# Performance work log

Hardware: AMD Instinct MI355X
Metric: run time of the kernel (lower is better)

The kernel has to match this reference:

```python
import jax, jax.numpy as jnp
import numpy as np

N_NODES = 200000
N_EDGES = 3200000
N_GRAPHS = 2000
N_MAX = 256   # max nodes per graph for dense batching (mean ~100)
K = 30        # SortAggregation k


def setup_inputs() -> dict:
    key = jax.random.key(0)
    ks = jax.random.split(key, 12)
    x = jax.random.normal(ks[0], (N_NODES, 128), jnp.float32)
    edge_index = jax.random.randint(ks[1], (2, N_EDGES), 0, N_NODES, dtype=jnp.int32)
    batch = jnp.sort(jax.random.randint(ks[2], (N_NODES,), 0, N_GRAPHS, dtype=jnp.int32))
    def lin(k, i, o):
        return (jax.random.normal(k, (i, o), jnp.float32) / np.sqrt(i)).astype(jnp.float32)
    return {
        'x': x, 'edge_index': edge_index, 'batch': batch,
        'W1': lin(ks[3], 128, 32), 'b1': jnp.zeros(32, jnp.float32),
        'W2': lin(ks[4], 32, 32),  'b2': jnp.zeros(32, jnp.float32),
        'W3': lin(ks[5], 32, 32),  'b3': jnp.zeros(32, jnp.float32),
        'W4': lin(ks[6], 32, 1),   'b4': jnp.zeros(1, jnp.float32),
        'cw5': (jax.random.normal(ks[7], (16, 1, 97), jnp.float32) / np.sqrt(97)).astype(jnp.float32),
        'cb5': jnp.zeros(16, jnp.float32),
        'cw6': (jax.random.normal(ks[8], (32, 16, 5), jnp.float32) / np.sqrt(80)).astype(jnp.float32),
        'cb6': jnp.zeros(32, jnp.float32),
        'fw1': lin(ks[9], 352, 128), 'fb1': jnp.zeros(128, jnp.float32),
        'fw2': lin(ks[10], 128, 10), 'fb2': jnp.zeros(10, jnp.float32),
    }


def _gcn_conv(h, W, b, src, dst, emask):
    # PyG GCNConv: remove self-loops handled via emask (weight 0), then add
    # self-loops weight 1; symmetric normalization D^{-1/2}(A+I)D^{-1/2} X W + b
    deg = jax.ops.segment_sum(emask, dst, num_segments=N_NODES) + 1.0  # + self loop
    dis = jax.lax.rsqrt(deg)  # deg >= 1 always, no inf
    norm = dis[src] * dis[dst] * emask  # [E]
    hw = h @ W                          # [N, out]
    agg = jax.ops.segment_sum(hw[src] * norm[:, None], dst, num_segments=N_NODES)
    agg = agg + hw * (dis * dis)[:, None]  # self-loop message
    return agg + b


def _sort_pool(x, batch):
    # PyG SortAggregation(k): dense-batch with fill = min-1, sort each graph by
    # last feature channel (descending), keep top-k rows, zero out padding, flatten.
    N, D = x.shape
    ones = jnp.ones((N,), jnp.int32)
    counts = jax.ops.segment_sum(ones, batch, num_segments=N_GRAPHS)
    offsets = jnp.concatenate([jnp.zeros((1,), jnp.int32), jnp.cumsum(counts)[:-1]])
    pos = jnp.arange(N, dtype=jnp.int32) - offsets[batch]  # batch is sorted
    fill = x.min() - 1.0
    dense = jnp.full((N_GRAPHS, N_MAX, D), fill, x.dtype).at[batch, pos].set(x)
    perm = jnp.argsort(-dense[:, :, -1], axis=1)            # descending by last channel
    dense = jnp.take_along_axis(dense, perm[:, :, None], axis=1)[:, :K]  # [G, K, D]
    dense = jnp.where(dense == fill, 0.0, dense)
    return dense.reshape(N_GRAPHS, K * D)


def _conv1d(x, w, b, stride):
    y = jax.lax.conv_general_dilated(x, w, window_strides=(stride,), padding='VALID',
                                     dimension_numbers=('NCH', 'OIH', 'NCH'))
    return y + b[None, :, None]


def reference(x, edge_index, batch, W1, b1, W2, b2, W3, b3, W4, b4,
              cw5, cb5, cw6, cb6, fw1, fb1, fw2, fb2):
    src, dst = edge_index[0], edge_index[1]
    emask = (src != dst).astype(x.dtype)  # remove_self_loops

    x1 = jnp.tanh(_gcn_conv(x,  W1, b1, src, dst, emask))
    x2 = jnp.tanh(_gcn_conv(x1, W2, b2, src, dst, emask))
    x3 = jnp.tanh(_gcn_conv(x2, W3, b3, src, dst, emask))
    x4 = jnp.tanh(_gcn_conv(x3, W4, b4, src, dst, emask))
    h = jnp.concatenate([x1, x2, x3, x4], axis=-1)  # [N, 97]

    p = _sort_pool(h, batch)                 # [G, 30*97]
    p = p[:, None, :]                        # [G, 1, 2910]
    p = jax.nn.relu(_conv1d(p, cw5, cb5, 97))  # [G, 16, 30]
    G = p.shape[0]
    p = p.reshape(G, 16, 15, 2).max(axis=-1)   # MaxPool1d(2,2) -> [G, 16, 15]
    p = jax.nn.relu(_conv1d(p, cw6, cb6, 1))   # [G, 32, 11]
    p = p.reshape(G, -1)                       # [G, 352]
    out = jax.nn.relu(p @ fw1 + fb1)           # dropout is identity at inference
    return jax.nn.log_softmax(out @ fw2 + fb2, axis=-1)
```

## Files before the change

### kernel.cpp

```cpp
#include <hip/hip_runtime.h>

#define N_NODESC 200000
#define N_EDGESC 3200000
#define N_GRAPHSC 2000
#define NMAXG 256
#define TOPK 30
#define DCAT 97
#define POOLW (TOPK*DCAT)
#define BUCKW 512
#define NBUCK ((N_NODESC+BUCKW-1)/BUCKW)
#define CAP 10240
#define PCHUNK 4096
#define NPBLK ((N_EDGESC+PCHUNK-1)/PCHUNK)

typedef int  iv4 __attribute__((ext_vector_type(4)));
typedef float fv4 __attribute__((ext_vector_type(4)));

__global__ __launch_bounds__(256) void k_part(const int* __restrict__ src, const int* __restrict__ dst,
                                              const int* __restrict__ batch, int* __restrict__ gcount,
                                              int* __restrict__ bcur, unsigned* __restrict__ pairbuf){
  __shared__ int hcnt[NBUCK];
  __shared__ int hbase[NBUCK];
  int blk = blockIdx.x, t = threadIdx.x;
  int nd = blk*256 + t;
  if (nd < N_NODESC) atomicAdd(&gcount[batch[nd]],1);
  int e0 = blk*PCHUNK;
  int e1 = e0 + PCHUNK; if (e1 > N_EDGESC) e1 = N_EDGESC;
  for (int i=t;i<NBUCK;i+=256) hcnt[i]=0;
  unsigned pk[16]; unsigned meta[16];
  __syncthreads();
  #pragma unroll
  for (int i=0;i<4;i++){
    int e = e0 + i*1024 + t*4;
    if (e < e1){
      iv4 d4 = __builtin_nontemporal_load((const iv4*)(dst+e));
      iv4 s4 = __builtin_nontemporal_load((const iv4*)(src+e));
      #pragma unroll
      for (int k=0;k<4;k++){
        int d = (k==0)?d4.x:(k==1)?d4.y:(k==2)?d4.z:d4.w;
        int s = (k==0)?s4.x:(k==1)?s4.y:(k==2)?s4.z:s4.w;
        if (s!=d){
          int bk = d>>9;
          int pl = atomicAdd(&hcnt[bk],1);
          pk[i*4+k]   = ((unsigned)(d&511)<<18)|(unsigned)s;
          meta[i*4+k] = ((unsigned)bk<<13)|(unsigned)pl;
        } else meta[i*4+k] = 0xFFFFFFFFu;
      }
    } else {
      #pragma unroll
      for (int k=0;k<4;k++) meta[i*4+k] = 0xFFFFFFFFu;
    }
  }
  __syncthreads();
  for (int i=t;i<NBUCK;i+=256){
    int c = hcnt[i];
    hbase[i] = c ? (i*CAP + atomicAdd(&bcur[i],c)) : 0;
  }
  __syncthreads();
  #pragma unroll
  for (int k=0;k<16;k++){
    unsigned m = meta[k];
    if (m != 0xFFFFFFFFu){
      int bk = (int)(m>>13);
      int pos = hbase[bk] + (int)(m & 0x1FFFu);
      if (pos < (bk+1)*CAP) pairbuf[pos] = pk[k];
    }
  }
}

__global__ __launch_bounds__(512) void k_bsort(const unsigned* __restrict__ pairbuf, const int* __restrict__ bcur,
                                               int* __restrict__ degc, int* __restrict__ offs,
                                               float* __restrict__ dis, int* __restrict__ csr){
  __shared__ int lcsr[CAP];
  __shared__ int lcnt[512];
  __shared__ int lofs[512];
  __shared__ int lcur[512];
  __shared__ int red[512];
  int b = blockIdx.x, t = threadIdx.x;
  int cnt_b = bcur[b]; if (cnt_b > CAP) cnt_b = CAP;
  int pv = 0;
  if (t < b){ int c = bcur[t]; if (c>CAP) c=CAP; pv = c; }
  red[t]=pv; __syncthreads();
  for (int off=256;off>0;off>>=1){ if (t<off) red[t]+=red[t+off]; __syncthreads(); }
  int base = red[0];
  const unsigned* pb = pairbuf + (size_t)b*CAP;
  lcnt[t]=0; __syncthreads();
  for (int i=t;i<cnt_b;i+=512) atomicAdd(&lcnt[pb[i]>>18],1);
  __syncthreads();
  lofs[t]=lcnt[t]; __syncthreads();
  for (int off=1;off<512;off<<=1){
    int u = (t>=off)? lofs[t-off] : 0;
    __syncthreads();
    lofs[t]+=u;
    __syncthreads();
  }
  int excl = lofs[t]-lcnt[t];
  int node = b*BUCKW + t;
  if (node < N_NODESC){
    degc[node] = lcnt[t];
    offs[node] = base + excl;
    dis[node]  = rsqrtf((float)lcnt[t] + 1.0f);
  }
  lcur[t]=excl;
  __syncthreads();
  for (int i=t;i<cnt_b;i+=512){
    unsigned v = pb[i];
    int p = atomicAdd(&lcur[v>>18],1);
    lcsr[p] = (int)(v & 0x3FFFFu);
  }
  __syncthreads();
  for (int i=t;i<cnt_b;i+=512) csr[base+i]=lcsr[i];
}

template<int KIN>
__global__ __launch_bounds__(256) void k_mm(const float* __restrict__ X, const float* __restrict__ W,
                                            const float* __restrict__ dis, float* __restrict__ out){
  __shared__ float xs[256*33];
  int r0 = blockIdx.x*256;
  int t = threadIdx.x;
  int r = r0 + t;
  float acc[32];
  #pragma unroll
  for (int f=0;f<32;f++) acc[f]=0.f;
  for (int kc=0; kc<KIN; kc+=32){
    __syncthreads();
    #pragma unroll
    for (int it=0; it<8; it++){
      int idx = it*256 + t;
      int row = idx>>3, c4 = idx&7;
      int gr = r0 + row;
      fv4 v = {0.f,0.f,0.f,0.f};
      if (gr < N_NODESC) v = __builtin_nontemporal_load((const fv4*)(X + (size_t)gr*KIN + kc + c4*4));
      int bofs = row*33 + c4*4;
      xs[bofs]=v.x; xs[bofs+1]=v.y; xs[bofs+2]=v.z; xs[bofs+3]=v.w;
    }
    __syncthreads();
    const float* w0 = W + kc*32;
    const float* xrow = xs + t*33;
    #pragma unroll
    for (int k=0;k<32;k++){
      float xv = xrow[k];
      #pragma unroll
      for (int f=0;f<32;f++) acc[f] = fmaf(xv, w0[k*32+f], acc[f]);
    }
  }
  if (r >= N_NODESC) return;
  float d = dis[r];
  float4* op = (float4*)(out + (size_t)r*32);
  #pragma unroll
  for (int f4=0;f4<8;f4++)
    op[f4] = make_float4(acc[4*f4]*d, acc[4*f4+1]*d, acc[4*f4+2]*d, acc[4*f4+3]*d);
}

__global__ void k_mm4(const float* __restrict__ X, const float* __restrict__ W, const float* __restrict__ dis, float* __restrict__ out){
  int r = blockIdx.x*256+threadIdx.x;
  if (r>=N_NODESC) return;
  const float4* xr = (const float4*)(X + (size_t)r*32);
  float acc=0.f;
  #pragma unroll
  for (int k4=0;k4<8;k4++){
    float4 xv = xr[k4];
    acc = fmaf(xv.x, W[k4*4+0], acc);
    acc = fmaf(xv.y, W[k4*4+1], acc);
    acc = fmaf(xv.z, W[k4*4+2], acc);
    acc = fmaf(xv.w, W[k4*4+3], acc);
  }
  out[r]=acc*dis[r];
}

__global__ __launch_bounds__(256) void k_agg(const float* __restrict__ hws, const int* __restrict__ csr,
                      const int* __restrict__ off, const int* __restrict__ cnt,
                      const float* __restrict__ dis, const float* __restrict__ bias,
                      float* __restrict__ out){
  int t = blockIdx.x*256 + threadIdx.x;
  int n = t>>5;
  if (n>=N_NODESC) return;
  int f = t&31;
  int beg = off[n], c = cnt[n];
  float a0=0.f,a1=0.f,a2=0.f,a3=0.f,a4=0.f,a5=0.f,a6=0.f,a7=0.f;
  for (int base=0; base<c; base+=32){
    int m = c-base; if (m>32) m=32;
    int idx = (f<m)? csr[beg+base+f] : 0;
    int j=0;
    for (; j+8<=m; j+=8){
      int s0=__shfl(idx,j,32),   s1=__shfl(idx,j+1,32),
          s2=__shfl(idx,j+2,32), s3=__shfl(idx,j+3,32),
          s4=__shfl(idx,j+4,32), s5=__shfl(idx,j+5,32),
          s6=__shfl(idx,j+6,32), s7=__shfl(idx,j+7,32);
      float v0=hws[(size_t)s0*32+f];
      float v1=hws[(size_t)s1*32+f];
      float v2=hws[(size_t)s2*32+f];
      float v3=hws[(size_t)s3*32+f];
      float v4=hws[(size_t)s4*32+f];
      float v5=hws[(size_t)s5*32+f];
      float v6=hws[(size_t)s6*32+f];
      float v7=hws[(size_t)s7*32+f];
      a0+=v0; a1+=v1; a2+=v2; a3+=v3; a4+=v4; a5+=v5; a6+=v6; a7+=v7;
    }
    for (; j+4<=m; j+=4){
      int s0=__shfl(idx,j,32), s1=__shfl(idx,j+1,32),
          s2=__shfl(idx,j+2,32), s3=__shfl(idx,j+3,32);
      float v0=hws[(size_t)s0*32+f];
      float v1=hws[(size_t)s1*32+f];
      float v2=hws[(size_t)s2*32+f];
      float v3=hws[(size_t)s3*32+f];
      a0+=v0; a1+=v1; a2+=v2; a3+=v3;
    }
    for (; j<m; j++){
      int s0=__shfl(idx,j,32);
      a0 += hws[(size_t)s0*32+f];
    }
  }
  float dn = dis[n];
  float sum = ((a0+a1)+(a2+a3)) + ((a4+a5)+(a6+a7));
  float v = dn*(sum+hws[(size_t)n*32+f]) + bias[f];
  out[(size_t)n*32+f] = tanhf(v);
}

__global__ void k_agg4(const float* __restrict__ hws4, const int* __restrict__ csr,
                       const int* __restrict__ off, const int* __restrict__ cnt,
                       const float* __restrict__ dis, const float* __restrict__ b4,
                       float* __restrict__ x4){
  int n = blockIdx.x*256+threadIdx.x;
  if (n>=N_NODESC) return;
  int beg=off[n], c=cnt[n];
  float a0=0.f,a1=0.f,a2=0.f,a3=0.f,a4=0.f,a5=0.f,a6=0.f,a7=0.f;
  int e=0;
  for (; e+8<=c; e+=8){
    int s0=csr[beg+e],   s1=csr[beg+e+1], s2=csr[beg+e+2], s3=csr[beg+e+3];
    int s4=csr[beg+e+4], s5=csr[beg+e+5], s6=csr[beg+e+6], s7=csr[beg+e+7];
    a0+=hws4[s0]; a1+=hws4[s1]; a2+=hws4[s2]; a3+=hws4[s3];
    a4+=hws4[s4]; a5+=hws4[s5]; a6+=hws4[s6]; a7+=hws4[s7];
  }
  for (; e<c; e++) a0+=hws4[csr[beg+e]];
  float dn=dis[n];
  float sum = ((a0+a1)+(a2+a3)) + ((a4+a5)+(a6+a7));
  x4[n] = tanhf(dn*(sum+hws4[n]) + b4[0]);
}

__global__ __launch_bounds__(256) void k_sortpool(const float* __restrict__ x1,const float* __restrict__ x2,const float* __restrict__ x3,const float* __restrict__ x4,
                           const int* __restrict__ gcount, float* __restrict__ pool){
  __shared__ float vals[NMAXG];
  __shared__ int sel[TOPK];
  __shared__ int redsum[256];
  int g = blockIdx.x;
  int t = threadIdx.x;
  int part = 0;
  for (int i=t; i<g; i+=256) part += gcount[i];
  redsum[t]=part; __syncthreads();
  for (int off=128;off>0;off>>=1){ if (t<off) redsum[t]+=redsum[t+off]; __syncthreads(); }
  int start = redsum[0];
  int cntg = gcount[g]; if (cntg>NMAXG) cntg=NMAXG;
  float v = 0.f;
  if (t<cntg) v = x4[start+t];
  vals[t] = v;
  __syncthreads();
  if (t<cntg){
    int rank=0;
    for (int j=0;j<cntg;j++){
      float vj=vals[j];
      rank += (vj>v) || (vj==v && j<t);
    }
    if (rank<TOPK) sel[rank]=t;
  }
  __syncthreads();
  int nsel = cntg<TOPK?cntg:TOPK;
  float* pg = pool + (size_t)g*POOLW;
  for (int idx=t; idx<POOLW; idx+=256){
    int r = idx/DCAT, c = idx - r*DCAT;
    float val=0.f;
    if (r<nsel){
      int node = start + sel[r];
      if (c<32) val = x1[(size_t)node*32+c];
      else if (c<64) val = x2[(size_t)node*32+(c-32)];
      else if (c<96) val = x3[(size_t)node*32+(c-64)];
      else val = x4[node];
    }
    pg[idx]=val;
  }
}

__global__ __launch_bounds__(128) void k_head(const float* __restrict__ pool,
                       const float* __restrict__ cw5, const float* __restrict__ cb5,
                       const float* __restrict__ cw6, const float* __restrict__ cb6,
                       const float* __restrict__ fw1, const float* __restrict__ fb1,
                       const float* __restrict__ fw2, const float* __restrict__ fb2,
                       float* __restrict__ out){
  __shared__ float P[POOLW];
  __shared__ float o5[16*30];
  __shared__ float m[16*15];
  __shared__ float o6[32*11];
  __shared__ float o1[128];
  __shared__ float logits[10];
  int g=blockIdx.x, t=threadIdx.x;
  const float* pg = pool + (size_t)g*POOLW;
  for (int i=t;i<POOLW;i+=128) P[i]=pg[i];
  __syncthreads();
  for (int i=t;i<480;i+=128){
    int o=i/30, k=i-o*30;
    float acc=cb5[o];
    const float* w=cw5+o*97;
    const float* p=P+k*97;
    for(int c=0;c<97;c++) acc = fmaf(p[c], w[c], acc);
    o5[o*30+k]=fmaxf(acc,0.f);
  }
  __syncthreads();
  for (int i=t;i<240;i+=128){
    int o=i/15,k=i-o*15;
    m[i]=fmaxf(o5[o*30+2*k], o5[o*30+2*k+1]);
  }
  __syncthreads();
  for (int i=t;i<352;i+=128){
    int o2=i/11, k=i-o2*11;
    float acc=cb6[o2];
    const float* w=cw6+o2*80;
    #pragma unroll
    for(int ii=0;ii<16;ii++)
      #pragma unroll
      for(int r=0;r<5;r++)
        acc = fmaf(m[ii*15+k+r], w[ii*5+r], acc);
    o6[o2*11+k]=fmaxf(acc,0.f);
  }
  __syncthreads();
  {
    float acc=fb1[t];
    for(int i=0;i<352;i++) acc = fmaf(o6[i], fw1[i*128+t], acc);
    o1[t]=fmaxf(acc,0.f);
  }
  __syncthreads();
  if (t<10){
    float acc=fb2[t];
    for(int j=0;j<128;j++) acc = fmaf(o1[j], fw2[j*10+t], acc);
    logits[t]=acc;
  }
  __syncthreads();
  if (t==0){
    float mx=logits[0];
    for(int c=1;c<10;c++) mx=fmaxf(mx,logits[c]);
    float s=0.f;
    for(int c=0;c<10;c++) s+=expf(logits[c]-mx);
    float lse=logf(s)+mx;
    for(int c=0;c<10;c++) out[(size_t)g*10+c]=logits[c]-lse;
  }
}

extern "C" void kernel_launch(void* const* d_in, const int* in_sizes, int n_in,
                              void* d_out, int out_size, void* d_ws, size_t ws_size,
                              hipStream_t stream){
  const float* x    = (const float*)d_in[0];
  const int*   ei   = (const int*)d_in[1];
  const int*   batch= (const int*)d_in[2];
  const float* W1=(const float*)d_in[3]; const float* b1=(const float*)d_in[4];
  const float* W2=(const float*)d_in[5]; const float* b2=(const float*)d_in[6];
  const float* W3=(const float*)d_in[7]; const float* b3=(const float*)d_in[8];
  const float* W4=(const float*)d_in[9]; const float* b4=(const float*)d_in[10];
  const float* cw5=(const float*)d_in[11]; const float* cb5=(const float*)d_in[12];
  const float* cw6=(const float*)d_in[13]; const float* cb6=(const float*)d_in[14];
  const float* fw1=(const float*)d_in[15]; const float* fb1=(const float*)d_in[16];
  const float* fw2=(const float*)d_in[17]; const float* fb2=(const float*)d_in[18];
  float* out=(float*)d_out;
  const int* src = ei;
  const int* dst = ei + N_EDGESC;

  char* ws=(char*)d_ws;
  size_t o=0;
  auto alloc=[&](size_t nbytes)->char*{ char* p=ws+o; o += (nbytes+255)&~(size_t)255; return p; };
  float* dis    = (float*)alloc((size_t)N_NODESC*4);
  int*   offs   = (int*)alloc((size_t)N_NODESC*4);
  int*   degc   = (int*)alloc((size_t)N_NODESC*4);
  int*   bcur   = (int*)alloc((size_t)NBUCK*4);
  int*   gcount = (int*)alloc((size_t)N_GRAPHSC*4);
  unsigned* pairbuf = (unsigned*)alloc((size_t)NBUCK*CAP*4);
  int*   csr    = (int*)alloc((size_t)N_EDGESC*4);
  float* x1 = (float*)alloc((size_t)N_NODESC*32*4);
  float* x2 = (float*)alloc((size_t)N_NODESC*32*4);
  float* x3 = (float*)alloc((size_t)N_NODESC*32*4);
  float* x4 = (float*)alloc((size_t)N_NODESC*4);
  float* hw = (float*)alloc((size_t)N_NODESC*32*4);
  float* pool = hw;

  size_t mset = (((size_t)NBUCK*4+255)&~(size_t)255) + (size_t)N_GRAPHSC*4;
  (void)hipMemsetAsync(bcur, 0, mset, stream);

  int gN = (N_NODESC+255)/256;

  k_part<<<NPBLK,256,0,stream>>>(src,dst,batch,gcount,bcur,pairbuf);
  k_bsort<<<NBUCK,512,0,stream>>>(pairbuf,bcur,degc,offs,dis,csr);

  int gMM=(N_NODESC+7)/8;
  k_mm<128><<<gN,256,0,stream>>>(x, W1, dis, hw);
  k_agg<<<gMM,256,0,stream>>>(hw,csr,offs,degc,dis,b1,x1);
  k_mm<32><<<gN,256,0,stream>>>(x1, W2, dis, hw);
  k_agg<<<gMM,256,0,stream>>>(hw,csr,offs,degc,dis,b2,x2);
  k_mm<32><<<gN,256,0,stream>>>(x2, W3, dis, hw);
  k_agg<<<gMM,256,0,stream>>>(hw,csr,offs,degc,dis,b3,x3);
  k_mm4<<<gN,256,0,stream>>>(x3, W4, dis, hw);
  k_agg4<<<gN,256,0,stream>>>(hw,csr,offs,degc,dis,b4,x4);

  k_sortpool<<<N_GRAPHSC,256,0,stream>>>(x1,x2,x3,x4,gcount,pool);
  k_head<<<N_GRAPHSC,128,0,stream>>>(pool,cw5,cb5,cw6,cb6,fw1,fb1,fw2,fb2,out);
}
```

Before: 485.9 us.

## Stage partitioned edges in LDS for coalesced writes; fuse layer-4 matvec into agg

The partition kernel now does an exclusive scan over per-bucket counts and stages each block's edge pairs in shared memory, sorted by bucket. It then writes them to global memory contiguously per bucket instead of scattering individual stores. Separately, the layer-3 aggregation kernel now also computes the 32-to-1 layer-4 projection with a wave reduction. This removes the k_mm4 launch and the re-read of x3. The cost is about 24KB more LDS in k_part, which may lower occupancy, plus extra scan synchronisation.

```diff
diff --git a/kernel.cpp b/kernel.cpp
--- a/kernel.cpp
+++ b/kernel.cpp
@@ -21,6 +21,10 @@
                                               int* __restrict__ bcur, unsigned* __restrict__ pairbuf){
   __shared__ int hcnt[NBUCK];
   __shared__ int hbase[NBUCK];
+  __shared__ int lofs[NBUCK];
+  __shared__ int scan[256];
+  __shared__ unsigned lbuf[PCHUNK];
+  __shared__ unsigned short bbuf[PCHUNK];
   int blk = blockIdx.x, t = threadIdx.x;
   int nd = blk*256 + t;
   if (nd < N_NODESC) atomicAdd(&gcount[batch[nd]],1);
@@ -52,6 +56,20 @@
     }
   }
   __syncthreads();
+  int i0=2*t, i1=2*t+1;
+  int h0 = (i0<NBUCK)? hcnt[i0] : 0;
+  int h1 = (i1<NBUCK)? hcnt[i1] : 0;
+  int sp = h0+h1;
+  scan[t]=sp; __syncthreads();
+  for (int off=1;off<256;off<<=1){
+    int u = (t>=off)? scan[t-off] : 0;
+    __syncthreads();
+    scan[t]+=u;
+    __syncthreads();
+  }
+  int ex = scan[t]-sp;
+  if (i0<NBUCK) lofs[i0]=ex;
+  if (i1<NBUCK) lofs[i1]=ex+h0;
   for (int i=t;i<NBUCK;i+=256){
     int c = hcnt[i];
     hbase[i] = c ? (i*CAP + atomicAdd(&bcur[i],c)) : 0;
@@ -62,9 +80,17 @@
     unsigned m = meta[k];
     if (m != 0xFFFFFFFFu){
       int bk = (int)(m>>13);
-      int pos = hbase[bk] + (int)(m & 0x1FFFu);
-      if (pos < (bk+1)*CAP) pairbuf[pos] = pk[k];
-    }
+      int j = lofs[bk] + (int)(m & 0x1FFFu);
+      lbuf[j] = pk[k];
+      bbuf[j] = (unsigned short)bk;
+    }
+  }
+  __syncthreads();
+  int tot = lofs[NBUCK-1] + hcnt[NBUCK-1];
+  for (int j=t; j<tot; j+=256){
+    int bk = bbuf[j];
+    int addr = hbase[bk] + (j - lofs[bk]);
+    if (addr < (bk+1)*CAP) pairbuf[addr] = lbuf[j];
   }
 }
 
@@ -150,22 +176,6 @@
   #pragma unroll
   for (int f4=0;f4<8;f4++)
     op[f4] = make_float4(acc[4*f4]*d, acc[4*f4+1]*d, acc[4*f4+2]*d, acc[4*f4+3]*d);
-}
-
-__global__ void k_mm4(const float* __restrict__ X, const float* __restrict__ W, const float* __restrict__ dis, float* __restrict__ out){
-  int r = blockIdx.x*256+threadIdx.x;
-  if (r>=N_NODESC) return;
-  const float4* xr = (const float4*)(X + (size_t)r*32);
-  float acc=0.f;
-  #pragma unroll
-  for (int k4=0;k4<8;k4++){
-    float4 xv = xr[k4];
-    acc = fmaf(xv.x, W[k4*4+0], acc);
-    acc = fmaf(xv.y, W[k4*4+1], acc);
-    acc = fmaf(xv.z, W[k4*4+2], acc);
-    acc = fmaf(xv.w, W[k4*4+3], acc);
-  }
-  out[r]=acc*dis[r];
 }
 
 __global__ __launch_bounds__(256) void k_agg(const float* __restrict__ hws, const int* __restrict__ csr,
@@ -217,6 +227,64 @@
   out[(size_t)n*32+f] = tanhf(v);
 }
 
+__global__ __launch_bounds__(256) void k_aggF1(const float* __restrict__ hws, const int* __restrict__ csr,
+                      const int* __restrict__ off, const int* __restrict__ cnt,
+                      const float* __restrict__ dis, const float* __restrict__ bias,
+                      const float* __restrict__ W4,
+                      float* __restrict__ xout, float* __restrict__ hw4){
+  __shared__ float Ws[32];
+  int t = threadIdx.x;
+  if (t<32) Ws[t]=W4[t];
+  __syncthreads();
+  int gt = blockIdx.x*256 + t;
+  int n = gt>>5;
+  if (n>=N_NODESC) return;
+  int f = gt&31;
+  int beg = off[n], c = cnt[n];
+  float a0=0.f,a1=0.f,a2=0.f,a3=0.f,a4=0.f,a5=0.f,a6=0.f,a7=0.f;
+  for (int base=0; base<c; base+=32){
+    int m = c-base; if (m>32) m=32;
+    int idx = (f<m)? csr[beg+base+f] : 0;
+    int j=0;
+    for (; j+8<=m; j+=8){
+      int s0=__shfl(idx,j,32),   s1=__shfl(idx,j+1,32),
+          s2=__shfl(idx,j+2,32), s3=__shfl(idx,j+3,32),
+          s4=__shfl(idx,j+4,32), s5=__shfl(idx,j+5,32),
+          s6=__shfl(idx,j+6,32), s7=__shfl(idx,j+7,32);
+      float v0=hws[(size_t)s0*32+f];
+      float v1=hws[(size_t)s1*32+f];
+      float v2=hws[(size_t)s2*32+f];
+      float v3=hws[(size_t)s3*32+f];
+      float v4=hws[(size_t)s4*32+f];
+      float v5=hws[(size_t)s5*32+f];
+      float v6=hws[(size_t)s6*32+f];
+      float v7=hws[(size_t)s7*32+f];
+      a0+=v0; a1+=v1; a2+=v2; a3+=v3; a4+=v4; a5+=v5; a6+=v6; a7+=v7;
+    }
+    for (; j+4<=m; j+=4){
+      int s0=__shfl(idx,j,32), s1=__shfl(idx,j+1,32),
+          s2=__shfl(idx,j+2,32), s3=__shfl(idx,j+3,32);
+      float v0=hws[(size_t)s0*32+f];
+      float v1=hws[(size_t)s1*32+f];
+      float v2=hws[(size_t)s2*32+f];
+      float v3=hws[(size_t)s3*32+f];
+      a0+=v0; a1+=v1; a2+=v2; a3+=v3;
+    }
+    for (; j<m; j++){
+      int s0=__shfl(idx,j,32);
+      a0 += hws[(size_t)s0*32+f];
+    }
+  }
+  float dn = dis[n];
+  float sum = ((a0+a1)+(a2+a3)) + ((a4+a5)+(a6+a7));
+  float xv = tanhf(dn*(sum+hws[(size_t)n*32+f]) + bias[f]);
+  xout[(size_t)n*32+f] = xv;
+  float acc = xv*Ws[f];
+  #pragma unroll
+  for (int off2=16;off2>0;off2>>=1) acc += __shfl_xor(acc, off2, 32);
+  if (f==0) hw4[n] = acc*dn;
+}
+
 __global__ void k_agg4(const float* __restrict__ hws4, const int* __restrict__ csr,
                        const int* __restrict__ off, const int* __restrict__ cnt,
                        const float* __restrict__ dis, const float* __restrict__ b4,
@@ -377,6 +445,7 @@
   float* x3 = (float*)alloc((size_t)N_NODESC*32*4);
   float* x4 = (float*)alloc((size_t)N_NODESC*4);
   float* hw = (float*)alloc((size_t)N_NODESC*32*4);
+  float* hw4 = (float*)alloc((size_t)N_NODESC*4);
   float* pool = hw;
 
   size_t mset = (((size_t)NBUCK*4+255)&~(size_t)255) + (size_t)N_GRAPHSC*4;
@@ -393,9 +462,8 @@
   k_mm<32><<<gN,256,0,stream>>>(x1, W2, dis, hw);
   k_agg<<<gMM,256,0,stream>>>(hw,csr,offs,degc,dis,b2,x2);
   k_mm<32><<<gN,256,0,stream>>>(x2, W3, dis, hw);
-  k_agg<<<gMM,256,0,stream>>>(hw,csr,offs,degc,dis,b3,x3);
-  k_mm4<<<gN,256,0,stream>>>(x3, W4, dis, hw);
-  k_agg4<<<gN,256,0,stream>>>(hw,csr,offs,degc,dis,b4,x4);
+  k_aggF1<<<gMM,256,0,stream>>>(hw,csr,offs,degc,dis,b3,W4,x3,hw4);
+  k_agg4<<<gN,256,0,stream>>>(hw4,csr,offs,degc,dis,b4,x4);
 
   k_sortpool<<<N_GRAPHSC,256,0,stream>>>(x1,x2,x3,x4,gcount,pool);
   k_head<<<N_GRAPHSC,128,0,stream>>>(pool,cw5,cb5,cw6,cb6,fw1,fb1,fw2,fb2,out);
```

New measurement: 477.8 us. No clear change (-1.7%).
